# Kernel tuning notes

Measured on AMD Instinct MI355X. Metric: run time of the kernel, lower is better.

The kernel has to match this reference:

```python
import jax, jax.numpy as jnp
import numpy as np

NUM_USERS = 100000
NUM_ITEMS = 50000
EMBED_DIM = 64
NNZ = 4_000_000
BATCH = 4096
N_LAYERS = 3
WEIGHT_DECAY = 1e-4


def setup_inputs() -> dict:
    key = jax.random.key(0)
    ks = jax.random.split(key, 8)
    N = NUM_USERS + NUM_ITEMS
    user_emb = 0.1 * jax.random.normal(ks[0], (NUM_USERS, EMBED_DIM), dtype=jnp.float32)
    item_emb = 0.1 * jax.random.normal(ks[1], (NUM_ITEMS, EMBED_DIM), dtype=jnp.float32)
    graph_rows = jax.random.randint(ks[2], (NNZ,), 0, N, dtype=jnp.int32)
    graph_cols = jax.random.randint(ks[3], (NNZ,), 0, N, dtype=jnp.int32)
    # normalized-adjacency-like small positive values
    graph_vals = 0.05 * jax.random.uniform(ks[4], (NNZ,), dtype=jnp.float32)
    users = jax.random.randint(ks[5], (BATCH,), 0, NUM_USERS, dtype=jnp.int32)
    positive_items = jax.random.randint(ks[6], (BATCH,), 0, NUM_ITEMS, dtype=jnp.int32)
    negative_items = jax.random.randint(ks[7], (BATCH,), 0, NUM_ITEMS, dtype=jnp.int32)
    return {
        "user_emb": user_emb,
        "item_emb": item_emb,
        "graph_rows": graph_rows,
        "graph_cols": graph_cols,
        "graph_vals": graph_vals,
        "users": users,
        "positive_items": positive_items,
        "negative_items": negative_items,
    }


def _spmm(rows, cols, vals, x, n):
    # sparse (n,n) @ x[n,d] via gather + segment_sum
    return jax.ops.segment_sum(vals[:, None] * x[cols], rows, num_segments=n)


def reference(user_emb, item_emb, graph_rows, graph_cols, graph_vals,
              users, positive_items, negative_items):
    N = user_emb.shape[0] + item_emb.shape[0]
    all_e = jnp.concatenate([user_emb, item_emb], axis=0)  # [N, D]
    acc = all_e
    cur = all_e
    for _ in range(N_LAYERS):
        cur = _spmm(graph_rows, graph_cols, graph_vals, cur, N)
        acc = acc + cur
    light_out = acc / jnp.float32(N_LAYERS + 1)  # mean over stacked layers

    nu = user_emb.shape[0]
    u_e = light_out[users]
    p_e = light_out[nu + positive_items]
    n_e = light_out[nu + negative_items]

    u_o = user_emb[users]
    p_o = item_emb[positive_items]
    n_o = item_emb[negative_items]

    B = users.shape[0]
    regular = 0.5 * (jnp.sum(u_o ** 2) + jnp.sum(p_o ** 2) + jnp.sum(n_o ** 2)) / jnp.float32(B)
    pos_s = jnp.sum(u_e * p_e, axis=1)
    neg_s = jnp.sum(u_e * n_e, axis=1)
    loss = jnp.mean(jax.nn.softplus(neg_s - pos_s)) + WEIGHT_DECAY * regular
    return loss
```

## Files before the change

### kernel.cpp

```cpp
#include <hip/hip_runtime.h>
#include <math.h>

#define NU 100000
#define NI 50000
#define NT 150000
#define D  64
#define NNZ_ 4000000
#define BATCH_ 4096
#define WDECAY 1e-4f

#define BROWS 2048
#define NBKT 74
#define BCAP 57344
#define CURS 16
#define EPB 16
#define BATCH_E (256 * EPB)
#define NBLK_A ((NNZ_ + BATCH_E - 1) / BATCH_E)

static __device__ __forceinline__ float bf2f(ushort u) {
    return __uint_as_float(((unsigned int)u) << 16);
}
static __device__ __forceinline__ ushort f2bf(float f) {
    unsigned int u = __float_as_uint(f);
    u += 0x7FFF + ((u >> 16) & 1);
    return (ushort)(u >> 16);
}

__global__ void init_kernel(const float* __restrict__ ue, const float* __restrict__ ie,
                            ushort* __restrict__ cur0, float* __restrict__ scal) {
    int i = blockIdx.x * blockDim.x + threadIdx.x;
    const int total4 = NT * D / 4;
    if (i == 0) { scal[0] = 0.f; scal[1] = 0.f; }
    if (i >= total4) return;
    const int usz4 = NU * D / 4;
    float4 v = (i < usz4) ? ((const float4*)ue)[i] : ((const float4*)ie)[i - usz4];
    ushort4 o;
    o.x = f2bf(v.x); o.y = f2bf(v.y); o.z = f2bf(v.z); o.w = f2bf(v.w);
    ((ushort4*)cur0)[i] = o;
}

__global__ void binA_kernel(const int* __restrict__ rows, const int* __restrict__ cols,
                            const float* __restrict__ vals,
                            int* __restrict__ cursor, int2* __restrict__ binned) {
    __shared__ int cnt[NBKT];
    __shared__ int gbase[NBKT];
    int tid = threadIdx.x;
    int b0 = blockIdx.x * BATCH_E;
    if (tid < NBKT) cnt[tid] = 0;
    __syncthreads();
    int pack[EPB];
    #pragma unroll
    for (int k = 0; k < EPB; ++k) {
        int i = b0 + k * 256 + tid;
        if (i < NNZ_) {
            int r = rows[i];
            int b = r >> 11;
            int rk = atomicAdd(&cnt[b], 1);
            pack[k] = (r & (BROWS - 1)) | (b << 11) | (rk << 18);
        } else pack[k] = -1;
    }
    __syncthreads();
    if (tid < NBKT) {
        int c = cnt[tid];
        gbase[tid] = c ? atomicAdd(&cursor[tid * CURS], c) : 0;
    }
    __syncthreads();
    #pragma unroll
    for (int k = 0; k < EPB; ++k) {
        int pk = pack[k];
        if (pk >= 0) {
            int i  = b0 + k * 256 + tid;
            int rl = pk & (BROWS - 1);
            int b  = (pk >> 11) & 127;
            int rk = pk >> 18;
            int2 e;
            e.x = rl | (cols[i] << 11);
            e.y = __float_as_int(vals[i]);
            binned[(size_t)b * BCAP + gbase[b] + rk] = e;
        }
    }
}

__global__ void bscan_kernel(const int* __restrict__ cursor, int* __restrict__ bbase,
                             int* __restrict__ rowptr) {
    __shared__ int s[128];
    int t = threadIdx.x;
    int v = (t < NBKT) ? cursor[t * CURS] : 0;
    s[t] = v; __syncthreads();
    for (int off = 1; off < 128; off <<= 1) {
        int x = (t >= off) ? s[t - off] : 0;
        __syncthreads();
        s[t] += x;
        __syncthreads();
    }
    if (t < NBKT) bbase[t] = s[t] - v;
    if (t == 0) rowptr[NT] = NNZ_;
}

__global__ void binB_kernel(const int2* __restrict__ binned, const int* __restrict__ cursor,
                            const int* __restrict__ bbase,
                            int2* __restrict__ colval, int* __restrict__ rowptr) {
    __shared__ int cnt[BROWS];
    __shared__ int sc[1024];
    __shared__ int offs[BROWS];
    int b   = blockIdx.x;
    int tid = threadIdx.x;
    int cb  = cursor[b * CURS];
    int base = bbase[b];
    const int2* eb = binned + (size_t)b * BCAP;
    cnt[tid] = 0; cnt[tid + 1024] = 0;
    __syncthreads();
    for (int i = tid; i < cb; i += 1024)
        atomicAdd(&cnt[eb[i].x & (BROWS - 1)], 1);
    __syncthreads();
    int v0 = cnt[2 * tid], v1 = cnt[2 * tid + 1];
    sc[tid] = v0 + v1;
    __syncthreads();
    for (int off = 1; off < 1024; off <<= 1) {
        int x = (tid >= off) ? sc[tid - off] : 0;
        __syncthreads();
        sc[tid] += x;
        __syncthreads();
    }
    int pbase = sc[tid] - (v0 + v1);
    offs[2 * tid]     = pbase;
    offs[2 * tid + 1] = pbase + v0;
    int row0 = b * BROWS + 2 * tid;
    if (row0 < NT)     rowptr[row0]     = base + pbase;
    if (row0 + 1 < NT) rowptr[row0 + 1] = base + pbase + v0;
    __syncthreads();
    for (int i = tid; i < cb; i += 1024) {
        int2 e = eb[i];
        int rl = e.x & (BROWS - 1);
        int p  = base + atomicAdd(&offs[rl], 1);
        int2 cv; cv.x = e.x >> 11; cv.y = e.y;
        colval[p] = cv;
    }
}

static __device__ __forceinline__ void row_core(const int* __restrict__ rowptr,
                                                const int2* __restrict__ colval,
                                                const ushort* __restrict__ x,
                                                int r, int lane,
                                                float& s0, float& s1, float& s2, float& s3) {
    int q  = lane >> 4;
    int ql = lane & 15;
    int beg = rowptr[r], end = rowptr[r + 1];
    s0 = s1 = s2 = s3 = 0.f;
    for (int base = beg; base < end; base += 64) {
        int m = end - base; if (m > 64) m = 64;
        int idx = base + lane; if (idx > NNZ_ - 1) idx = NNZ_ - 1;
        int2 cv = colval[idx];
        int nq = (m + 3) >> 2;
        #pragma unroll 4
        for (int j = 0; j < nq; ++j) {
            int e = 4 * j + q;
            int   c = __shfl(cv.x, e);
            float v = __int_as_float(__shfl(cv.y, e));
            if (e >= m) v = 0.f;
            ushort4 xv = *(const ushort4*)(x + (size_t)c * D + ql * 4);
            s0 += v * bf2f(xv.x); s1 += v * bf2f(xv.y);
            s2 += v * bf2f(xv.z); s3 += v * bf2f(xv.w);
        }
    }
    s0 += __shfl_xor(s0, 16); s0 += __shfl_xor(s0, 32);
    s1 += __shfl_xor(s1, 16); s1 += __shfl_xor(s1, 32);
    s2 += __shfl_xor(s2, 16); s2 += __shfl_xor(s2, 32);
    s3 += __shfl_xor(s3, 16); s3 += __shfl_xor(s3, 32);
}

__global__ void spmm_kernel(const int* __restrict__ rowptr, const int2* __restrict__ colval,
                            const ushort* __restrict__ x, ushort* __restrict__ y) {
    int gtid = blockIdx.x * blockDim.x + threadIdx.x;
    int r    = gtid >> 6;
    int lane = threadIdx.x & 63;
    if (r >= NT) return;
    float s0, s1, s2, s3;
    row_core(rowptr, colval, x, r, lane, s0, s1, s2, s3);
    if ((lane >> 4) == 0) {
        int ql = lane & 15;
        ushort4 o;
        o.x = f2bf(s0); o.y = f2bf(s1); o.z = f2bf(s2); o.w = f2bf(s3);
        *(ushort4*)(y + (size_t)r * D + ql * 4) = o;
    }
}

static __device__ __forceinline__ float row_walk(const int* __restrict__ rowptr,
                                                 const int2* __restrict__ colval,
                                                 const ushort* __restrict__ x,
                                                 int r, int lane) {
    float s0, s1, s2, s3;
    row_core(rowptr, colval, x, r, lane, s0, s1, s2, s3);
    int srcl = lane >> 2;
    float w0 = __shfl(s0, srcl), w1 = __shfl(s1, srcl);
    float w2 = __shfl(s2, srcl), w3 = __shfl(s3, srcl);
    int sel = lane & 3;
    return sel == 0 ? w0 : sel == 1 ? w1 : sel == 2 ? w2 : w3;
}

__global__ void loss_kernel(const float* __restrict__ ue, const float* __restrict__ ie,
                            const ushort* __restrict__ o1, const ushort* __restrict__ o2,
                            const int* __restrict__ rowptr, const int2* __restrict__ colval,
                            const int* __restrict__ users, const int* __restrict__ pos,
                            const int* __restrict__ neg, float* __restrict__ scal) {
    int gtid = blockIdx.x * blockDim.x + threadIdx.x;
    int wid  = gtid >> 6;
    int lane = threadIdx.x & 63;
    int nw   = (gridDim.x * blockDim.x) >> 6;
    for (int b = wid; b < BATCH_; b += nw) {
        int u = users[b], p = pos[b], n = neg[b];
        int ru = u, rp = NU + p, rn = NU + n;
        float uo = ue[(size_t)u * D + lane];
        float po = ie[(size_t)p * D + lane];
        float no = ie[(size_t)n * D + lane];
        float lu = uo + bf2f(o1[(size_t)ru * D + lane]) + bf2f(o2[(size_t)ru * D + lane])
                      + row_walk(rowptr, colval, o2, ru, lane);
        float lp = po + bf2f(o1[(size_t)rp * D + lane]) + bf2f(o2[(size_t)rp * D + lane])
                      + row_walk(rowptr, colval, o2, rp, lane);
        float ln_ = no + bf2f(o1[(size_t)rn * D + lane]) + bf2f(o2[(size_t)rn * D + lane])
                      + row_walk(rowptr, colval, o2, rn, lane);
        float ps = lu * lp;
        float ns = lu * ln_;
        float rg = uo * uo + po * po + no * no;
        #pragma unroll
        for (int off = 32; off > 0; off >>= 1) {
            ps += __shfl_down(ps, off);
            ns += __shfl_down(ns, off);
            rg += __shfl_down(rg, off);
        }
        if (lane == 0) {
            float diff = (ns - ps) * (1.0f / 16.0f);
            float sp = diff > 0.f ? diff + log1pf(expf(-diff)) : log1pf(expf(diff));
            atomicAdd(&scal[0], sp);
            atomicAdd(&scal[1], rg);
        }
    }
}

__global__ void finalize_kernel(const float* __restrict__ scal, float* __restrict__ out) {
    out[0] = scal[0] / (float)BATCH_ + WDECAY * 0.5f * scal[1] / (float)BATCH_;
}

extern "C" void kernel_launch(void* const* d_in, const int* in_sizes, int n_in,
                              void* d_out, int out_size, void* d_ws, size_t ws_size,
                              hipStream_t stream) {
    const float* user_emb = (const float*)d_in[0];
    const float* item_emb = (const float*)d_in[1];
    const int*   g_rows   = (const int*)d_in[2];
    const int*   g_cols   = (const int*)d_in[3];
    const float* g_vals   = (const float*)d_in[4];
    const int*   users    = (const int*)d_in[5];
    const int*   pos      = (const int*)d_in[6];
    const int*   neg      = (const int*)d_in[7];
    float* out = (float*)d_out;

    const size_t TABH = (size_t)NT * D * 2;
    char* ws = (char*)d_ws;
    ushort* cur0   = (ushort*)(ws);
    ushort* o1     = (ushort*)(ws + TABH);
    ushort* o2     = (ushort*)(ws + 2 * TABH);
    int2*   colval = (int2*)  (ws + 3 * TABH);
    int2*   binned = (int2*)  (ws + 3 * TABH + (size_t)NNZ_ * 8);
    char*   p      = ws + 3 * TABH + (size_t)NNZ_ * 8 + (size_t)NBKT * BCAP * 8;
    int*    rowptr = (int*)(p);      p += ((size_t)(NT + 1) * 4 + 255) / 256 * 256;
    int*    cursor = (int*)(p);      p += (size_t)NBKT * CURS * 4;
    int*    bbase  = (int*)(p);      p += 1024;
    float*  scal   = (float*)(p);

    hipMemsetAsync(cursor, 0, (size_t)NBKT * CURS * 4, stream);
    init_kernel<<<(NT * D / 4 + 255) / 256, 256, 0, stream>>>(user_emb, item_emb, cur0, scal);

    binA_kernel<<<NBLK_A, 256, 0, stream>>>(g_rows, g_cols, g_vals, cursor, binned);
    bscan_kernel<<<1, 128, 0, stream>>>(cursor, bbase, rowptr);
    binB_kernel<<<NBKT, 1024, 0, stream>>>(binned, cursor, bbase, colval, rowptr);

    const int SPMM_BLOCKS = (NT + 3) / 4;
    spmm_kernel<<<SPMM_BLOCKS, 256, 0, stream>>>(rowptr, colval, cur0, o1);
    spmm_kernel<<<SPMM_BLOCKS, 256, 0, stream>>>(rowptr, colval, o1, o2);

    loss_kernel<<<1024, 256, 0, stream>>>(user_emb, item_emb, o1, o2, rowptr, colval,
                                          users, pos, neg, scal);
    finalize_kernel<<<1, 1, 0, stream>>>(scal, out);
}
```

Measured before the change: 567.4 us.

## Split final-layer row walks into separate kernel and raise inner unroll

The third-layer SpMM rows needed for the batch (user, positive, negative) are now computed by a dedicated walk_kernel with one wavefront per row task, 12288 tasks in all, writing fp32 results to a workspace buffer. Previously each loss wavefront walked all three rows one after another. The loss kernel now just reads those buffers and uses fewer blocks. The SpMM inner loop unroll also goes from 4 to 8 to get more gathers in flight. The split adds a kernel launch and a small buffer round trip through memory.

```diff
diff --git a/kernel.cpp b/kernel.cpp
--- a/kernel.cpp
+++ b/kernel.cpp
@@ -152,7 +152,7 @@
         int idx = base + lane; if (idx > NNZ_ - 1) idx = NNZ_ - 1;
         int2 cv = colval[idx];
         int nq = (m + 3) >> 2;
-        #pragma unroll 4
+        #pragma unroll 8
         for (int j = 0; j < nq; ++j) {
             int e = 4 * j + q;
             int   c = __shfl(cv.x, e);
@@ -185,22 +185,29 @@
     }
 }
 
-static __device__ __forceinline__ float row_walk(const int* __restrict__ rowptr,
-                                                 const int2* __restrict__ colval,
-                                                 const ushort* __restrict__ x,
-                                                 int r, int lane) {
+__global__ void walk_kernel(const ushort* __restrict__ o2,
+                            const int* __restrict__ rowptr, const int2* __restrict__ colval,
+                            const int* __restrict__ users, const int* __restrict__ pos,
+                            const int* __restrict__ neg, float* __restrict__ wbuf) {
+    int gtid = blockIdx.x * blockDim.x + threadIdx.x;
+    int task = gtid >> 6;
+    int lane = threadIdx.x & 63;
+    if (task >= 3 * BATCH_) return;
+    int role = task >> 12;
+    int b    = task & (BATCH_ - 1);
+    int r = (role == 0) ? users[b] : (role == 1) ? NU + pos[b] : NU + neg[b];
     float s0, s1, s2, s3;
-    row_core(rowptr, colval, x, r, lane, s0, s1, s2, s3);
-    int srcl = lane >> 2;
-    float w0 = __shfl(s0, srcl), w1 = __shfl(s1, srcl);
-    float w2 = __shfl(s2, srcl), w3 = __shfl(s3, srcl);
-    int sel = lane & 3;
-    return sel == 0 ? w0 : sel == 1 ? w1 : sel == 2 ? w2 : w3;
+    row_core(rowptr, colval, o2, r, lane, s0, s1, s2, s3);
+    if ((lane >> 4) == 0) {
+        int ql = lane & 15;
+        float4 o; o.x = s0; o.y = s1; o.z = s2; o.w = s3;
+        *(float4*)(wbuf + (size_t)task * D + ql * 4) = o;
+    }
 }
 
 __global__ void loss_kernel(const float* __restrict__ ue, const float* __restrict__ ie,
                             const ushort* __restrict__ o1, const ushort* __restrict__ o2,
-                            const int* __restrict__ rowptr, const int2* __restrict__ colval,
+                            const float* __restrict__ wbuf,
                             const int* __restrict__ users, const int* __restrict__ pos,
                             const int* __restrict__ neg, float* __restrict__ scal) {
     int gtid = blockIdx.x * blockDim.x + threadIdx.x;
@@ -214,11 +221,11 @@
         float po = ie[(size_t)p * D + lane];
         float no = ie[(size_t)n * D + lane];
         float lu = uo + bf2f(o1[(size_t)ru * D + lane]) + bf2f(o2[(size_t)ru * D + lane])
-                      + row_walk(rowptr, colval, o2, ru, lane);
+                      + wbuf[(size_t)(0 * BATCH_ + b) * D + lane];
         float lp = po + bf2f(o1[(size_t)rp * D + lane]) + bf2f(o2[(size_t)rp * D + lane])
-                      + row_walk(rowptr, colval, o2, rp, lane);
+                      + wbuf[(size_t)(1 * BATCH_ + b) * D + lane];
         float ln_ = no + bf2f(o1[(size_t)rn * D + lane]) + bf2f(o2[(size_t)rn * D + lane])
-                      + row_walk(rowptr, colval, o2, rn, lane);
+                      + wbuf[(size_t)(2 * BATCH_ + b) * D + lane];
         float ps = lu * lp;
         float ns = lu * ln_;
         float rg = uo * uo + po * po + no * no;
@@ -265,7 +272,8 @@
     int*    rowptr = (int*)(p);      p += ((size_t)(NT + 1) * 4 + 255) / 256 * 256;
     int*    cursor = (int*)(p);      p += (size_t)NBKT * CURS * 4;
     int*    bbase  = (int*)(p);      p += 1024;
-    float*  scal   = (float*)(p);
+    float*  scal   = (float*)(p);    p += 256;
+    float*  wbuf   = (float*)(p);
 
     hipMemsetAsync(cursor, 0, (size_t)NBKT * CURS * 4, stream);
     init_kernel<<<(NT * D / 4 + 255) / 256, 256, 0, stream>>>(user_emb, item_emb, cur0, scal);
@@ -278,7 +286,9 @@
     spmm_kernel<<<SPMM_BLOCKS, 256, 0, stream>>>(rowptr, colval, cur0, o1);
     spmm_kernel<<<SPMM_BLOCKS, 256, 0, stream>>>(rowptr, colval, o1, o2);
 
-    loss_kernel<<<1024, 256, 0, stream>>>(user_emb, item_emb, o1, o2, rowptr, colval,
-                                          users, pos, neg, scal);
+    walk_kernel<<<(3 * BATCH_ + 3) / 4, 256, 0, stream>>>(o2, rowptr, colval,
+                                                          users, pos, neg, wbuf);
+    loss_kernel<<<256, 256, 0, stream>>>(user_emb, item_emb, o1, o2, wbuf,
+                                         users, pos, neg, scal);
     finalize_kernel<<<1, 1, 0, stream>>>(scal, out);
 }
```

Result: no change. 575.1 us (+1.4%).
